# Kernel optimization log

Hardware: AMD Instinct MI355X
Metric: run time of the kernel (lower is better)

Reference implementation:

```python
import jax, jax.numpy as jnp
import numpy as np

B, S, H, I = 2, 1024, 1024, 4096
G, E = 4, 4
NE = G * E
CAP = 1024


def setup_inputs() -> dict:
    key = jax.random.key(0)
    ks = jax.random.split(key, 6)
    return {
        "hidden_states": jax.random.normal(ks[0], (B, S, H), jnp.float32),
        "group_router_w": jax.random.normal(ks[1], (G, H), jnp.float32) * 0.02,
        "expert_router_w": jax.random.normal(ks[2], (G, E, H), jnp.float32) * 0.02,
        "gate_w": jax.random.normal(ks[3], (NE, I, H), jnp.float32) * 0.02,
        "up_w": jax.random.normal(ks[4], (NE, I, H), jnp.float32) * 0.02,
        "down_w": jax.random.normal(ks[5], (NE, H, I), jnp.float32) * 0.02,
    }


def _forward(x, gw, erw, Wg, Wu, Wd):
    b, s, h = x.shape
    T = b * s
    xf = x.reshape(T, h)
    # level 1: group routing (fp32 softmax, top-2 groups)
    group_logits = xf @ gw.T                                        # [T,G]
    group_probs = jax.nn.softmax(group_logits.astype(jnp.float32), axis=-1)
    top_gp, top_gi = jax.lax.top_k(group_probs, 2)                  # [T,2]
    # level 2: per-group expert routing (top-1 expert within group)
    expert_logits = jnp.einsum('th,geh->tge', xf, erw)              # [T,G,E]
    expert_probs = jax.nn.softmax(expert_logits.astype(jnp.float32), axis=-1)
    e_idx = jnp.argmax(expert_probs, axis=-1)                       # [T,G]
    e_prob = jnp.max(expert_probs, axis=-1)                         # [T,G]
    sel_e = jnp.take_along_axis(e_idx, top_gi, axis=1)              # [T,2]
    sel_p = jnp.take_along_axis(e_prob, top_gi, axis=1)             # [T,2]
    eid = (top_gi * E + sel_e).reshape(-1)                          # [2T] global expert id
    wgt = (top_gp * sel_p).reshape(-1)                              # [2T] combine weight
    x2 = jnp.repeat(xf, 2, axis=0)                                  # [2T,H], slot-major per token
    # capacity-based dispatch: position within expert via cumsum of one-hot
    onehot = jax.nn.one_hot(eid, NE, dtype=jnp.int32)               # [2T,NE]
    pos = (jnp.cumsum(onehot, axis=0) * onehot).sum(axis=1) - 1     # [2T]
    keep = pos < CAP
    pos_c = jnp.where(keep, pos, CAP)                               # overflow -> dummy slot
    buf = jnp.zeros((NE, CAP + 1, h), x.dtype).at[eid, pos_c].set(x2)
    # grouped-GEMM gated FFN (SwiGLU) over all experts at once
    gate = jax.nn.silu(jnp.einsum('ech,eih->eci', buf, Wg))
    up = jnp.einsum('ech,eih->eci', buf, Wu)
    yexp = jnp.einsum('eci,ehi->ech', gate * up, Wd)                # [NE,CAP+1,H]
    # combine: gather back and weight; dropped tokens get zero weight
    y = yexp[eid, pos_c] * jnp.where(keep, wgt, 0.0)[:, None].astype(x.dtype)
    out = (y[0::2] + y[1::2]).reshape(b, s, h)
    aux_loss = jnp.zeros((), jnp.float32)  # aux-loss accumulation truncated in source; initialized to 0
    return out, aux_loss


def reference(hidden_states, group_router_w, expert_router_w, gate_w, up_w, down_w):
    return _forward(hidden_states, group_router_w, expert_router_w, gate_w, up_w, down_w)
```

## Files before the change

### kernel.cpp

```cpp
#include <hip/hip_runtime.h>
#include <hip/hip_bf16.h>

typedef float f32x4 __attribute__((ext_vector_type(4)));
typedef __bf16 bf16x8 __attribute__((ext_vector_type(8)));

#define H 1024
#define II 4096
#define NE 16
#define CAP 1024
#define NTOK 2048
#define NSLOT 4096

__device__ __forceinline__ void gload16(const void* g, void* l) {
  __builtin_amdgcn_global_load_lds(
      (const __attribute__((address_space(1))) unsigned*)g,
      (__attribute__((address_space(3))) unsigned*)l, 16, 0, 0);
}

__global__ __launch_bounds__(256) void k_route(
    const float* __restrict__ x, const float* __restrict__ gw,
    const float* __restrict__ erw, int* __restrict__ eid,
    float* __restrict__ wgt) {
  int t = blockIdx.x * 4 + (threadIdx.x >> 6);
  int lane = threadIdx.x & 63;
  const float* xr = x + (size_t)t * H;
  double acc[20];
#pragma unroll
  for (int j = 0; j < 20; j++) acc[j] = 0.0;
  for (int it = 0; it < 16; ++it) {
    int h = it * 64 + lane;
    float xv = xr[h];
#pragma unroll
    for (int g = 0; g < 4; ++g) acc[g] += (double)xv * (double)gw[g * H + h];
#pragma unroll
    for (int j = 0; j < 16; ++j)
      acc[4 + j] += (double)xv * (double)erw[j * H + h];
  }
#pragma unroll
  for (int j = 0; j < 20; ++j) {
    double v = acc[j];
#pragma unroll
    for (int o = 32; o > 0; o >>= 1) v += __shfl_down(v, o, 64);
    acc[j] = v;
  }
  if (lane == 0) {
    float gl[4];
#pragma unroll
    for (int g = 0; g < 4; g++) gl[g] = (float)acc[g];
    int g1 = 0;
#pragma unroll
    for (int g = 1; g < 4; g++)
      if (gl[g] > gl[g1]) g1 = g;
    int g2 = (g1 == 0) ? 1 : 0;
#pragma unroll
    for (int g = 0; g < 4; g++)
      if (g != g1 && gl[g] > gl[g2]) g2 = g;
    float gm = fmaxf(fmaxf(gl[0], gl[1]), fmaxf(gl[2], gl[3]));
    float s = 0.f;
#pragma unroll
    for (int g = 0; g < 4; g++) s += expf(gl[g] - gm);
    float p[2] = {expf(gl[g1] - gm) / s, expf(gl[g2] - gm) / s};
    int gs[2] = {g1, g2};
#pragma unroll
    for (int k = 0; k < 2; k++) {
      int g = gs[k];
      float el[4];
#pragma unroll
      for (int e2 = 0; e2 < 4; e2++) el[e2] = (float)acc[4 + g * 4 + e2];
      int eb = 0;
#pragma unroll
      for (int e2 = 1; e2 < 4; e2++)
        if (el[e2] > el[eb]) eb = e2;
      float es = 0.f;
#pragma unroll
      for (int e2 = 0; e2 < 4; e2++) es += expf(el[e2] - el[eb]);
      eid[2 * t + k] = g * 4 + eb;
      wgt[2 * t + k] = p[k] * (1.f / es);
    }
  }
}

__global__ __launch_bounds__(1024) void k_scan(const int* __restrict__ eid,
                                               int* __restrict__ perm,
                                               int* __restrict__ cnt,
                                               int* __restrict__ kept) {
  int wid = threadIdx.x >> 6;
  int lane = threadIdx.x & 63;
  int ne[64];
#pragma unroll
  for (int it = 0; it < 64; ++it) ne[it] = eid[it * 64 + lane];
  int base = 0;
#pragma unroll
  for (int it = 0; it < 64; ++it) {
    int slot = it * 64 + lane;
    int e = ne[it];
    unsigned long long m = __ballot(e == wid);
    if (e == wid) {
      int pos = base + __popcll(m & ((1ull << lane) - 1ull));
      if (pos < CAP) {
        perm[wid * CAP + pos] = slot;
        kept[slot] = 1;
      } else {
        kept[slot] = 0;
      }
    }
    base += __popcll(m);
  }
  if (lane == 0) cnt[wid] = (base < CAP) ? base : CAP;
}

__global__ __launch_bounds__(256) void k_cvtx(const float* __restrict__ x,
                                              __bf16* __restrict__ xb) {
  size_t i = ((size_t)blockIdx.x * 256 + threadIdx.x) * 8;
  f32x4 a = *(const f32x4*)(x + i);
  f32x4 b = *(const f32x4*)(x + i + 4);
  bf16x8 o;
#pragma unroll
  for (int j = 0; j < 4; j++) {
    o[j] = (__bf16)a[j];
    o[j + 4] = (__bf16)b[j];
  }
  *(bf16x8*)(xb + i) = o;
}

#define VMCNT(N) asm volatile("s_waitcnt vmcnt(" #N ")" ::: "memory")
#define LGK0 asm volatile("s_waitcnt lgkmcnt(0)" ::: "memory")
#define SBAR()                           \
  __builtin_amdgcn_sched_barrier(0);     \
  __builtin_amdgcn_s_barrier();          \
  __builtin_amdgcn_sched_barrier(0);

#define MFMA_BF16(A, B, C) __builtin_amdgcn_mfma_f32_16x16x32_bf16(A, B, C, 0, 0, 0)

__global__ __launch_bounds__(256, 3) void k_gateup(
    const __bf16* __restrict__ xb, const float* __restrict__ Wg,
    const float* __restrict__ Wu, const int* __restrict__ perm,
    const int* __restrict__ cnt, __bf16* __restrict__ act) {
  __shared__ __bf16 As[2][128 * 32];
  __shared__ float Gs[2][64 * 32];
  __shared__ float Us[2][64 * 32];
  __shared__ int slotArr[128];
  const int e = blockIdx.z, nt = blockIdx.x, rt = blockIdx.y;
  const int ce = cnt[e];
  if (ce <= 0 || rt * 128 >= ce) return;
  const int tid = threadIdx.x, lane = tid & 63, w = tid >> 6;
  if (tid < 128) {
    int ridx = rt * 128 + tid;
    slotArr[tid] = perm[e * CAP + (ridx < ce ? ridx : 0)];
  }
  __syncthreads();
  const int rA0 = 32 * w + (lane >> 2), rA1 = rA0 + 16;
  const __bf16* gA0 =
      xb + (size_t)(slotArr[rA0] >> 1) * H + (((lane & 3) ^ ((rA0 >> 1) & 3)) * 8);
  const __bf16* gA1 =
      xb + (size_t)(slotArr[rA1] >> 1) * H + (((lane & 3) ^ ((rA1 >> 1) & 3)) * 8);
  const int rW0 = 16 * w + (lane >> 3), rW1 = rW0 + 8;
  const size_t ew = (size_t)e * II * H + (size_t)(nt * 64) * H;
  const float* gG0 = Wg + ew + (size_t)rW0 * H + (((lane & 7) ^ (rW0 & 7)) * 4);
  const float* gG1 = Wg + ew + (size_t)rW1 * H + (((lane & 7) ^ (rW1 & 7)) * 4);
  const float* gU0 = Wu + ew + (size_t)rW0 * H + (((lane & 7) ^ (rW0 & 7)) * 4);
  const float* gU1 = Wu + ew + (size_t)rW1 * H + (((lane & 7) ^ (rW1 & 7)) * 4);
  const int wm = w >> 1, wn = w & 1;
  const int l15 = lane & 15, lk = lane >> 4;

  f32x4 accG[4][2], accU[4][2];
#pragma unroll
  for (int m = 0; m < 4; m++)
#pragma unroll
    for (int n = 0; n < 2; n++)
#pragma unroll
      for (int i = 0; i < 4; i++) {
        accG[m][n][i] = 0.f;
        accU[m][n][i] = 0.f;
      }

#define GU_STAGE(B, T)                                   \
  {                                                      \
    const int ko = (T) * 32;                             \
    gload16(gA0 + ko, &As[B][(32 * w) * 32]);            \
    gload16(gA1 + ko, &As[B][(32 * w + 16) * 32]);       \
    gload16(gG0 + ko, &Gs[B][(16 * w) * 32]);            \
    gload16(gG1 + ko, &Gs[B][(16 * w + 8) * 32]);        \
    gload16(gU0 + ko, &Us[B][(16 * w) * 32]);            \
    gload16(gU1 + ko, &Us[B][(16 * w + 8) * 32]);        \
  }
#define GU_COMPUTE(B)                                                       \
  {                                                                         \
    bf16x8 aF[4];                                                           \
    _Pragma("unroll") for (int m = 0; m < 4; m++) {                         \
      int r = wm * 64 + m * 16 + l15;                                       \
      aF[m] = *(const bf16x8*)&As[B][r * 32 + ((lk ^ ((r >> 1) & 3)) * 8)]; \
    }                                                                       \
    _Pragma("unroll") for (int n = 0; n < 2; n++) {                         \
      int r = wn * 32 + n * 16 + l15;                                       \
      int cA = (2 * lk) ^ (r & 7), cB = cA ^ 1;                             \
      f32x4 glo = *(const f32x4*)&Gs[B][r * 32 + cA * 4];                   \
      f32x4 ghi = *(const f32x4*)&Gs[B][r * 32 + cB * 4];                   \
      f32x4 ulo = *(const f32x4*)&Us[B][r * 32 + cA * 4];                   \
      f32x4 uhi = *(const f32x4*)&Us[B][r * 32 + cB * 4];                   \
      bf16x8 gF, uF;                                                        \
      _Pragma("unroll") for (int i = 0; i < 4; i++) {                       \
        gF[i] = (__bf16)glo[i];                                             \
        gF[i + 4] = (__bf16)ghi[i];                                         \
        uF[i] = (__bf16)ulo[i];                                             \
        uF[i + 4] = (__bf16)uhi[i];                                         \
      }                                                                     \
      _Pragma("unroll") for (int m = 0; m < 4; m++) {                       \
        accG[m][n] = MFMA_BF16(aF[m], gF, accG[m][n]);                      \
        accU[m][n] = MFMA_BF16(aF[m], uF, accU[m][n]);                      \
      }                                                                     \
    }                                                                       \
  }

  GU_STAGE(0, 0);
  GU_STAGE(1, 1);
  for (int t = 0; t < 31; ++t) {
    VMCNT(6);
    SBAR();
    GU_COMPUTE(t & 1);
    LGK0;
    SBAR();
    if (t + 2 < 32) GU_STAGE(t & 1, t + 2);
  }
  VMCNT(0);
  SBAR();
  GU_COMPUTE(1);

  const int colB = nt * 64 + wn * 32;
#pragma unroll
  for (int m = 0; m < 4; m++)
#pragma unroll
    for (int n = 0; n < 2; n++)
#pragma unroll
      for (int i = 0; i < 4; i++) {
        int row = wm * 64 + m * 16 + lk * 4 + i;
        if (rt * 128 + row < ce) {
          int slot = slotArr[row];
          float g = accG[m][n][i];
          float u = accU[m][n][i];
          float a = (g / (1.f + __expf(-g))) * u;
          act[(size_t)slot * II + colB + n * 16 + l15] = (__bf16)a;
        }
      }
}

__global__ __launch_bounds__(256, 4) void k_down(
    const __bf16* __restrict__ act, const float* __restrict__ Wd,
    const int* __restrict__ perm, const int* __restrict__ cnt,
    const float* __restrict__ wgt, float* __restrict__ yb0,
    float* __restrict__ yb1) {
  __shared__ __bf16 As[2][128 * 32];
  __shared__ float Ws[2][64 * 32];
  __shared__ int slotArr[128];
  const int e = blockIdx.z, nt = blockIdx.x;
  const int rt = blockIdx.y & 7, sk = blockIdx.y >> 3;
  const int ce = cnt[e];
  if (ce <= 0 || rt * 128 >= ce) return;
  const int tid = threadIdx.x, lane = tid & 63, w = tid >> 6;
  if (tid < 128) {
    int ridx = rt * 128 + tid;
    slotArr[tid] = perm[e * CAP + (ridx < ce ? ridx : 0)];
  }
  __syncthreads();
  const int KB = sk * 2048;
  const int rA0 = 32 * w + (lane >> 2), rA1 = rA0 + 16;
  const __bf16* gA0 =
      act + (size_t)slotArr[rA0] * II + KB + (((lane & 3) ^ ((rA0 >> 1) & 3)) * 8);
  const __bf16* gA1 =
      act + (size_t)slotArr[rA1] * II + KB + (((lane & 3) ^ ((rA1 >> 1) & 3)) * 8);
  const int rW0 = 16 * w + (lane >> 3), rW1 = rW0 + 8;
  const float* gW0 = Wd + (size_t)e * H * II + (size_t)(nt * 64 + rW0) * II + KB +
                     (((lane & 7) ^ (rW0 & 7)) * 4);
  const float* gW1 = Wd + (size_t)e * H * II + (size_t)(nt * 64 + rW1) * II + KB +
                     (((lane & 7) ^ (rW1 & 7)) * 4);
  const int wm = w >> 1, wn = w & 1;
  const int l15 = lane & 15, lk = lane >> 4;

  f32x4 acc[4][2];
#pragma unroll
  for (int m = 0; m < 4; m++)
#pragma unroll
    for (int n = 0; n < 2; n++)
#pragma unroll
      for (int i = 0; i < 4; i++) acc[m][n][i] = 0.f;

#define DN_STAGE(B, T)                                   \
  {                                                      \
    const int ko = (T) * 32;                             \
    gload16(gA0 + ko, &As[B][(32 * w) * 32]);            \
    gload16(gA1 + ko, &As[B][(32 * w + 16) * 32]);       \
    gload16(gW0 + ko, &Ws[B][(16 * w) * 32]);            \
    gload16(gW1 + ko, &Ws[B][(16 * w + 8) * 32]);        \
  }
#define DN_COMPUTE(B)                                                       \
  {                                                                         \
    bf16x8 aF[4];                                                           \
    _Pragma("unroll") for (int m = 0; m < 4; m++) {                         \
      int r = wm * 64 + m * 16 + l15;                                       \
      aF[m] = *(const bf16x8*)&As[B][r * 32 + ((lk ^ ((r >> 1) & 3)) * 8)]; \
    }                                                                       \
    _Pragma("unroll") for (int n = 0; n < 2; n++) {                         \
      int r = wn * 32 + n * 16 + l15;                                       \
      int cA = (2 * lk) ^ (r & 7), cB = cA ^ 1;                             \
      f32x4 wlo = *(const f32x4*)&Ws[B][r * 32 + cA * 4];                   \
      f32x4 whi = *(const f32x4*)&Ws[B][r * 32 + cB * 4];                   \
      bf16x8 wF;                                                            \
      _Pragma("unroll") for (int i = 0; i < 4; i++) {                       \
        wF[i] = (__bf16)wlo[i];                                             \
        wF[i + 4] = (__bf16)whi[i];                                         \
      }                                                                     \
      _Pragma("unroll") for (int m = 0; m < 4; m++)                         \
          acc[m][n] = MFMA_BF16(aF[m], wF, acc[m][n]);                      \
    }                                                                       \
  }

  DN_STAGE(0, 0);
  DN_STAGE(1, 1);
  for (int t = 0; t < 63; ++t) {
    VMCNT(4);
    SBAR();
    DN_COMPUTE(t & 1);
    LGK0;
    SBAR();
    if (t + 2 < 64) DN_STAGE(t & 1, t + 2);
  }
  VMCNT(0);
  SBAR();
  DN_COMPUTE(1);

  float* yp = sk ? yb1 : yb0;
  const int colB = nt * 64 + wn * 32;
#pragma unroll
  for (int m = 0; m < 4; m++)
#pragma unroll
    for (int n = 0; n < 2; n++)
#pragma unroll
      for (int i = 0; i < 4; i++) {
        int row = wm * 64 + m * 16 + lk * 4 + i;
        if (rt * 128 + row < ce) {
          int slot = slotArr[row];
          yp[(size_t)slot * H + colB + n * 16 + l15] =
              wgt[slot] * acc[m][n][i];
        }
      }
}

__global__ __launch_bounds__(256) void k_combine(const float* __restrict__ y0p,
                                                 const float* __restrict__ y1p,
                                                 const int* __restrict__ kept,
                                                 float* __restrict__ out) {
  int t = blockIdx.x, tid = threadIdx.x;
  size_t o0 = (size_t)(2 * t) * H, o1 = (size_t)(2 * t + 1) * H;
  f32x4 a, b;
#pragma unroll
  for (int i = 0; i < 4; i++) {
    a[i] = 0.f;
    b[i] = 0.f;
  }
  if (kept[2 * t])
    a = ((const f32x4*)(y0p + o0))[tid] + ((const f32x4*)(y1p + o0))[tid];
  if (kept[2 * t + 1])
    b = ((const f32x4*)(y0p + o1))[tid] + ((const f32x4*)(y1p + o1))[tid];
  ((f32x4*)out)[(size_t)t * 256 + tid] = a + b;
  if (t == 0 && tid == 0) out[(size_t)NTOK * H] = 0.f;
}

extern "C" void kernel_launch(void* const* d_in, const int* in_sizes, int n_in,
                              void* d_out, int out_size, void* d_ws,
                              size_t ws_size, hipStream_t stream) {
  const float* x = (const float*)d_in[0];
  const float* gw = (const float*)d_in[1];
  const float* erw = (const float*)d_in[2];
  const float* Wg = (const float*)d_in[3];
  const float* Wu = (const float*)d_in[4];
  const float* Wd = (const float*)d_in[5];
  float* out = (float*)d_out;
  char* ws = (char*)d_ws;
  int* eid = (int*)(ws);
  float* wgt = (float*)(ws + (16 << 10));
  int* kept = (int*)(ws + (32 << 10));
  int* cnt = (int*)(ws + (48 << 10));
  int* perm = (int*)(ws + (64 << 10));
  size_t off = 128 << 10;
  __bf16* act = (__bf16*)(ws + off);
  off += (size_t)NSLOT * II * 2;
  float* yb0 = (float*)(ws + off);
  off += (size_t)NSLOT * H * 4;
  float* yb1 = (float*)(ws + off);
  off += (size_t)NSLOT * H * 4;
  __bf16* xb = (__bf16*)(ws + off);

  k_route<<<NTOK / 4, 256, 0, stream>>>(x, gw, erw, eid, wgt);
  k_scan<<<1, 1024, 0, stream>>>(eid, perm, cnt, kept);
  k_cvtx<<<NTOK * H / 8 / 256, 256, 0, stream>>>(x, xb);
  k_gateup<<<dim3(64, 8, 16), 256, 0, stream>>>(xb, Wg, Wu, perm, cnt, act);
  k_down<<<dim3(16, 16, 16), 256, 0, stream>>>(act, Wd, perm, cnt, wgt, yb0, yb1);
  k_combine<<<NTOK, 256, 0, stream>>>(yb0, yb1, kept, out);
}
```

Baseline: 405.5 us.

## Double row tile to 256 with 512-thread blocks and 4-way split-K down

Both expert GEMM kernels now use 512-thread blocks covering 256 token rows, so each fp32 weight tile loaded into LDS is reused across twice as many rows. This halves repeated reads of the large weight matrices. The down projection switches to four K splits of 1024 with four partial output buffers, which the combine kernel sums. Costs are more wasted padded rows for lightly loaded experts, larger LDS per block, and extra partial-sum traffic in combine.

```diff
diff --git a/kernel.cpp b/kernel.cpp
--- a/kernel.cpp
+++ b/kernel.cpp
@@ -132,20 +132,20 @@
 
 #define MFMA_BF16(A, B, C) __builtin_amdgcn_mfma_f32_16x16x32_bf16(A, B, C, 0, 0, 0)
 
-__global__ __launch_bounds__(256, 3) void k_gateup(
+__global__ __launch_bounds__(512, 4) void k_gateup(
     const __bf16* __restrict__ xb, const float* __restrict__ Wg,
     const float* __restrict__ Wu, const int* __restrict__ perm,
     const int* __restrict__ cnt, __bf16* __restrict__ act) {
-  __shared__ __bf16 As[2][128 * 32];
+  __shared__ __bf16 As[2][256 * 32];
   __shared__ float Gs[2][64 * 32];
   __shared__ float Us[2][64 * 32];
-  __shared__ int slotArr[128];
+  __shared__ int slotArr[256];
   const int e = blockIdx.z, nt = blockIdx.x, rt = blockIdx.y;
   const int ce = cnt[e];
-  if (ce <= 0 || rt * 128 >= ce) return;
+  if (rt * 256 >= ce) return;
   const int tid = threadIdx.x, lane = tid & 63, w = tid >> 6;
-  if (tid < 128) {
-    int ridx = rt * 128 + tid;
+  if (tid < 256) {
+    int ridx = rt * 256 + tid;
     slotArr[tid] = perm[e * CAP + (ridx < ce ? ridx : 0)];
   }
   __syncthreads();
@@ -154,12 +154,10 @@
       xb + (size_t)(slotArr[rA0] >> 1) * H + (((lane & 3) ^ ((rA0 >> 1) & 3)) * 8);
   const __bf16* gA1 =
       xb + (size_t)(slotArr[rA1] >> 1) * H + (((lane & 3) ^ ((rA1 >> 1) & 3)) * 8);
-  const int rW0 = 16 * w + (lane >> 3), rW1 = rW0 + 8;
+  const int rW0 = 8 * w + (lane >> 3);
   const size_t ew = (size_t)e * II * H + (size_t)(nt * 64) * H;
   const float* gG0 = Wg + ew + (size_t)rW0 * H + (((lane & 7) ^ (rW0 & 7)) * 4);
-  const float* gG1 = Wg + ew + (size_t)rW1 * H + (((lane & 7) ^ (rW1 & 7)) * 4);
   const float* gU0 = Wu + ew + (size_t)rW0 * H + (((lane & 7) ^ (rW0 & 7)) * 4);
-  const float* gU1 = Wu + ew + (size_t)rW1 * H + (((lane & 7) ^ (rW1 & 7)) * 4);
   const int wm = w >> 1, wn = w & 1;
   const int l15 = lane & 15, lk = lane >> 4;
 
@@ -179,10 +177,8 @@
     const int ko = (T) * 32;                             \
     gload16(gA0 + ko, &As[B][(32 * w) * 32]);            \
     gload16(gA1 + ko, &As[B][(32 * w + 16) * 32]);       \
-    gload16(gG0 + ko, &Gs[B][(16 * w) * 32]);            \
-    gload16(gG1 + ko, &Gs[B][(16 * w + 8) * 32]);        \
-    gload16(gU0 + ko, &Us[B][(16 * w) * 32]);            \
-    gload16(gU1 + ko, &Us[B][(16 * w + 8) * 32]);        \
+    gload16(gG0 + ko, &Gs[B][(8 * w) * 32]);             \
+    gload16(gU0 + ko, &Us[B][(8 * w) * 32]);             \
   }
 #define GU_COMPUTE(B)                                                       \
   {                                                                         \
@@ -215,7 +211,7 @@
   GU_STAGE(0, 0);
   GU_STAGE(1, 1);
   for (int t = 0; t < 31; ++t) {
-    VMCNT(6);
+    VMCNT(4);
     SBAR();
     GU_COMPUTE(t & 1);
     LGK0;
@@ -234,7 +230,7 @@
 #pragma unroll
       for (int i = 0; i < 4; i++) {
         int row = wm * 64 + m * 16 + lk * 4 + i;
-        if (rt * 128 + row < ce) {
+        if (rt * 256 + row < ce) {
           int slot = slotArr[row];
           float g = accG[m][n][i];
           float u = accU[m][n][i];
@@ -244,35 +240,32 @@
       }
 }
 
-__global__ __launch_bounds__(256, 4) void k_down(
+__global__ __launch_bounds__(512, 6) void k_down(
     const __bf16* __restrict__ act, const float* __restrict__ Wd,
     const int* __restrict__ perm, const int* __restrict__ cnt,
-    const float* __restrict__ wgt, float* __restrict__ yb0,
-    float* __restrict__ yb1) {
-  __shared__ __bf16 As[2][128 * 32];
+    const float* __restrict__ wgt, float* __restrict__ yb) {
+  __shared__ __bf16 As[2][256 * 32];
   __shared__ float Ws[2][64 * 32];
-  __shared__ int slotArr[128];
+  __shared__ int slotArr[256];
   const int e = blockIdx.z, nt = blockIdx.x;
-  const int rt = blockIdx.y & 7, sk = blockIdx.y >> 3;
+  const int rt = blockIdx.y & 3, sk = blockIdx.y >> 2;
   const int ce = cnt[e];
-  if (ce <= 0 || rt * 128 >= ce) return;
+  if (rt * 256 >= ce) return;
   const int tid = threadIdx.x, lane = tid & 63, w = tid >> 6;
-  if (tid < 128) {
-    int ridx = rt * 128 + tid;
+  if (tid < 256) {
+    int ridx = rt * 256 + tid;
     slotArr[tid] = perm[e * CAP + (ridx < ce ? ridx : 0)];
   }
   __syncthreads();
-  const int KB = sk * 2048;
+  const int KB = sk * 1024;
   const int rA0 = 32 * w + (lane >> 2), rA1 = rA0 + 16;
   const __bf16* gA0 =
       act + (size_t)slotArr[rA0] * II + KB + (((lane & 3) ^ ((rA0 >> 1) & 3)) * 8);
   const __bf16* gA1 =
       act + (size_t)slotArr[rA1] * II + KB + (((lane & 3) ^ ((rA1 >> 1) & 3)) * 8);
-  const int rW0 = 16 * w + (lane >> 3), rW1 = rW0 + 8;
+  const int rW0 = 8 * w + (lane >> 3);
   const float* gW0 = Wd + (size_t)e * H * II + (size_t)(nt * 64 + rW0) * II + KB +
                      (((lane & 7) ^ (rW0 & 7)) * 4);
-  const float* gW1 = Wd + (size_t)e * H * II + (size_t)(nt * 64 + rW1) * II + KB +
-                     (((lane & 7) ^ (rW1 & 7)) * 4);
   const int wm = w >> 1, wn = w & 1;
   const int l15 = lane & 15, lk = lane >> 4;
 
@@ -289,8 +282,7 @@
     const int ko = (T) * 32;                             \
     gload16(gA0 + ko, &As[B][(32 * w) * 32]);            \
     gload16(gA1 + ko, &As[B][(32 * w + 16) * 32]);       \
-    gload16(gW0 + ko, &Ws[B][(16 * w) * 32]);            \
-    gload16(gW1 + ko, &Ws[B][(16 * w + 8) * 32]);        \
+    gload16(gW0 + ko, &Ws[B][(8 * w) * 32]);             \
   }
 #define DN_COMPUTE(B)                                                       \
   {                                                                         \
@@ -316,19 +308,19 @@
 
   DN_STAGE(0, 0);
   DN_STAGE(1, 1);
-  for (int t = 0; t < 63; ++t) {
-    VMCNT(4);
+  for (int t = 0; t < 31; ++t) {
+    VMCNT(3);
     SBAR();
     DN_COMPUTE(t & 1);
     LGK0;
     SBAR();
-    if (t + 2 < 64) DN_STAGE(t & 1, t + 2);
+    if (t + 2 < 32) DN_STAGE(t & 1, t + 2);
   }
   VMCNT(0);
   SBAR();
   DN_COMPUTE(1);
 
-  float* yp = sk ? yb1 : yb0;
+  float* yp = yb + (size_t)sk * NSLOT * H;
   const int colB = nt * 64 + wn * 32;
 #pragma unroll
   for (int m = 0; m < 4; m++)
@@ -337,7 +329,7 @@
 #pragma unroll
       for (int i = 0; i < 4; i++) {
         int row = wm * 64 + m * 16 + lk * 4 + i;
-        if (rt * 128 + row < ce) {
+        if (rt * 256 + row < ce) {
           int slot = slotArr[row];
           yp[(size_t)slot * H + colB + n * 16 + l15] =
               wgt[slot] * acc[m][n][i];
@@ -345,22 +337,26 @@
       }
 }
 
-__global__ __launch_bounds__(256) void k_combine(const float* __restrict__ y0p,
-                                                 const float* __restrict__ y1p,
+__global__ __launch_bounds__(256) void k_combine(const float* __restrict__ yb,
                                                  const int* __restrict__ kept,
                                                  float* __restrict__ out) {
   int t = blockIdx.x, tid = threadIdx.x;
   size_t o0 = (size_t)(2 * t) * H, o1 = (size_t)(2 * t + 1) * H;
+  const size_t ystride = (size_t)NSLOT * H;
   f32x4 a, b;
 #pragma unroll
   for (int i = 0; i < 4; i++) {
     a[i] = 0.f;
     b[i] = 0.f;
   }
-  if (kept[2 * t])
-    a = ((const f32x4*)(y0p + o0))[tid] + ((const f32x4*)(y1p + o0))[tid];
-  if (kept[2 * t + 1])
-    b = ((const f32x4*)(y0p + o1))[tid] + ((const f32x4*)(y1p + o1))[tid];
+  if (kept[2 * t]) {
+#pragma unroll
+    for (int s = 0; s < 4; s++) a = a + ((const f32x4*)(yb + s * ystride + o0))[tid];
+  }
+  if (kept[2 * t + 1]) {
+#pragma unroll
+    for (int s = 0; s < 4; s++) b = b + ((const f32x4*)(yb + s * ystride + o1))[tid];
+  }
   ((f32x4*)out)[(size_t)t * 256 + tid] = a + b;
   if (t == 0 && tid == 0) out[(size_t)NTOK * H] = 0.f;
 }
@@ -384,16 +380,14 @@
   size_t off = 128 << 10;
   __bf16* act = (__bf16*)(ws + off);
   off += (size_t)NSLOT * II * 2;
-  float* yb0 = (float*)(ws + off);
-  off += (size_t)NSLOT * H * 4;
-  float* yb1 = (float*)(ws + off);
-  off += (size_t)NSLOT * H * 4;
+  float* yb = (float*)(ws + off);
+  off += (size_t)4 * NSLOT * H * 4;
   __bf16* xb = (__bf16*)(ws + off);
 
   k_route<<<NTOK / 4, 256, 0, stream>>>(x, gw, erw, eid, wgt);
   k_scan<<<1, 1024, 0, stream>>>(eid, perm, cnt, kept);
   k_cvtx<<<NTOK * H / 8 / 256, 256, 0, stream>>>(x, xb);
-  k_gateup<<<dim3(64, 8, 16), 256, 0, stream>>>(xb, Wg, Wu, perm, cnt, act);
-  k_down<<<dim3(16, 16, 16), 256, 0, stream>>>(act, Wd, perm, cnt, wgt, yb0, yb1);
-  k_combine<<<NTOK, 256, 0, stream>>>(yb0, yb1, kept, out);
-}
+  k_gateup<<<dim3(64, 4, 16), 512, 0, stream>>>(xb, Wg, Wu, perm, cnt, act);
+  k_down<<<dim3(16, 16, 16), 512, 0, stream>>>(act, Wd, perm, cnt, wgt, yb);
+  k_combine<<<NTOK, 256, 0, stream>>>(yb, kept, out);
+}
```

New measurement: 441.4 us. 8.9% more time.
